# Kernel tuning notes

Measured on AMD Instinct MI355X. Metric: run time of the kernel, lower is better.

## Reference

```python
import jax, jax.numpy as jnp
import numpy as np

BATCH, SEQ, FEAT, UNITS, OUT = 128, 2048, 64, 64, 6


def setup_inputs() -> dict:
    key = jax.random.key(0)
    ks = jax.random.split(key, 12)
    s = 0.05
    inp = {
        "x": jax.random.normal(ks[0], (BATCH, SEQ, FEAT), dtype=jnp.float32),
        # LSTMCell 0 (kernel, recurrent_kernel, bias); gate order i,f,g,o
        "W0": jax.random.normal(ks[1], (FEAT, 4 * UNITS), dtype=jnp.float32) * s,
        "U0": jax.random.normal(ks[2], (UNITS, 4 * UNITS), dtype=jnp.float32) * s,
        "b0": jax.random.normal(ks[3], (4 * UNITS,), dtype=jnp.float32) * s,
        # LSTMCell 1 (shared by layers 2 AND 3, as in the original code)
        "W1": jax.random.normal(ks[4], (UNITS, 4 * UNITS), dtype=jnp.float32) * s,
        "U1": jax.random.normal(ks[5], (UNITS, 4 * UNITS), dtype=jnp.float32) * s,
        "b1": jax.random.normal(ks[6], (4 * UNITS,), dtype=jnp.float32) * s,
        # Dense heads
        "Wf": jax.random.normal(ks[7], (UNITS, 64), dtype=jnp.float32) * s,
        "bf": jax.random.normal(ks[8], (64,), dtype=jnp.float32) * s,
        "Wo": jax.random.normal(ks[9], (64, OUT), dtype=jnp.float32) * s,
        "bo": jax.random.normal(ks[10], (OUT,), dtype=jnp.float32) * s,
    }
    return inp


def _lstm_cell(c, h, xin, W, U, b):
    # Keras LSTMCell math, gate order i, f, g(candidate), o
    z = xin @ W + h @ U + b  # [B, 4U]
    i, f, g, o = jnp.split(z, 4, axis=-1)
    c_new = jax.nn.sigmoid(f) * c + jax.nn.sigmoid(i) * jnp.tanh(g)
    h_new = jax.nn.sigmoid(o) * jnp.tanh(c_new)
    return c_new, h_new


def reference(x, W0, U0, b0, W1, U1, b1, Wf, bf, Wo, bo):
    B = x.shape[0]
    z = jnp.zeros((B, UNITS), dtype=x.dtype)
    init = (z, z, z, z, z, z)  # (c0,h0,c1,h1,c2,h2)

    def step(carry, xt):
        c0, h0, c1, h1, c2, h2 = carry
        c0, h0 = _lstm_cell(c0, h0, xt, W0, U0, b0)
        c1, h1 = _lstm_cell(c1, h1, h0, W1, U1, b1)
        # NOTE: original code reuses rnn_cell1's weights for the 3rd layer
        c2, h2 = _lstm_cell(c2, h2, h1, W1, U1, b1)
        return (c0, h0, c1, h1, c2, h2), None

    xt = jnp.swapaxes(x, 0, 1)  # [T, B, F]
    (c0, h0, c1, h1, c2, h2), _ = jax.lax.scan(step, init, xt)
    y = jax.nn.relu(h2 @ Wf + bf)
    return y @ Wo + bo
```

## Files before the change

### kernel.cpp

```cpp
#include <hip/hip_runtime.h>

#define BATCHN 128
#define SEQT   2048
#define FEAT   64
#define UNITS  64
#define NCOL   256
#define OUTD   6

typedef float v2f __attribute__((ext_vector_type(2)));

__device__ __forceinline__ float fast_exp2(float x) {
#if __has_builtin(__builtin_amdgcn_exp2f)
    return __builtin_amdgcn_exp2f(x);
#else
    return exp2f(x);
#endif
}
__device__ __forceinline__ float fast_rcp(float x) {
#if __has_builtin(__builtin_amdgcn_rcpf)
    return __builtin_amdgcn_rcpf(x);
#else
    return 1.0f / x;
#endif
}
__device__ __forceinline__ float sig_(float x) {
    return fast_rcp(1.0f + fast_exp2(-1.4426950408889634f * x));
}
__device__ __forceinline__ float tanh_(float x) {
    float xc = fminf(fmaxf(x, -15.0f), 15.0f);
    float e  = fast_exp2(2.8853900817779268f * xc);
    return (e - 1.0f) * fast_rcp(e + 1.0f);
}

__device__ __forceinline__ v2f pk_fma(v2f a, v2f b, v2f c) {
    return __builtin_elementwise_fma(a, b, c);
}

template<int CTRL>
__device__ __forceinline__ float dppf(float v) {
    return __builtin_bit_cast(float, __builtin_amdgcn_update_dpp(
        0, __builtin_bit_cast(int, v), CTRL, 0xF, 0xF, true));
}
__device__ __forceinline__ float red4(float v) {
    v += dppf<0xB1>(v);
    v += dppf<0x4E>(v);
    return v;
}

__global__ __launch_bounds__(768, 3)
void lstm3_pipe3(const float* __restrict__ x,
                 const float* __restrict__ W0, const float* __restrict__ U0,
                 const float* __restrict__ b0,
                 const float* __restrict__ W1, const float* __restrict__ U1,
                 const float* __restrict__ b1,
                 const float* __restrict__ Wf, const float* __restrict__ bfv,
                 const float* __restrict__ Wo, const float* __restrict__ bov,
                 float* __restrict__ out)
{
    const int b   = blockIdx.x;
    const int tid = threadIdx.x;
    const int grp = tid >> 8;
    const int lt  = tid & 255;
    const int u   = lt >> 2;
    const int q   = lt & 3;

    __shared__ __align__(16) float lx[2][FEAT];
    __shared__ __align__(16) float lh[3][2][UNITS];
    __shared__ float lact[UNITS];

    const float* Wsel = (grp == 0) ? W0 : W1;
    const float* Usel = (grp == 0) ? U0 : U1;
    const float* bsel = (grp == 0) ? b0 : b1;

    v2f wa[4][8], wb[4][8];
    float bias[4];
#pragma unroll
    for (int g = 0; g < 4; ++g) {
        const int col = (g << 6) + u;
#pragma unroll
        for (int j = 0; j < 8; ++j) {
            const int r = q * 16 + 2 * j;
            wa[g][j] = (v2f){Wsel[r * NCOL + col], Wsel[(r + 1) * NCOL + col]};
            wb[g][j] = (v2f){Usel[r * NCOL + col], Usel[(r + 1) * NCOL + col]};
        }
        bias[g] = bsel[col];
    }

    if (tid < 3 * 2 * UNITS) ((float*)lh)[tid] = 0.f;
    const float* xbase = x + (size_t)b * SEQT * FEAT;
    const bool xload = (grp == 0) && (lt < 16);
    if (xload)
        *(float4*)&lx[1][lt * 4] = *(const float4*)(xbase + lt * 4);
    __syncthreads();

    const float* inP0 = (grp == 0) ? &lx[0][q * 16] : &lh[grp - 1][0][q * 16];
    const float* inP1 = (grp == 0) ? &lx[1][q * 16] : &lh[grp - 1][1][q * 16];
    const float* rcP0 = &lh[grp][0][q * 16];
    const float* rcP1 = &lh[grp][1][q * 16];

    float c = 0.f;

    for (int tk = 0; tk < SEQT + 2; ++tk) {
        const int p = tk & 1;
        const int t = tk - grp;
        const bool active = (t >= 0) && (t < SEQT);

        float4 xg;
        const bool loading = xload && (tk + 1 < SEQT);
        if (loading)
            xg = *(const float4*)(xbase + (size_t)(tk + 1) * FEAT + lt * 4);

        if (active) {
            const float* inP = p ? inP0 : inP1;
            const float* rcP = p ? rcP0 : rcP1;

            v2f acc[4];
#pragma unroll
            for (int g = 0; g < 4; ++g) acc[g] = (v2f){0.f, 0.f};

#pragma unroll
            for (int kc = 0; kc < 4; ++kc) {
                float4 iv = *(const float4*)(inP + kc * 4);
                v2f i0 = (v2f){iv.x, iv.y}, i1 = (v2f){iv.z, iv.w};
#pragma unroll
                for (int g = 0; g < 4; ++g) {
                    acc[g] = pk_fma(i0, wa[g][2 * kc],     acc[g]);
                    acc[g] = pk_fma(i1, wa[g][2 * kc + 1], acc[g]);
                }
            }
#pragma unroll
            for (int kc = 0; kc < 4; ++kc) {
                float4 rv = *(const float4*)(rcP + kc * 4);
                v2f r0 = (v2f){rv.x, rv.y}, r1 = (v2f){rv.z, rv.w};
#pragma unroll
                for (int g = 0; g < 4; ++g) {
                    acc[g] = pk_fma(r0, wb[g][2 * kc],     acc[g]);
                    acc[g] = pk_fma(r1, wb[g][2 * kc + 1], acc[g]);
                }
            }

            float z[4];
#pragma unroll
            for (int g = 0; g < 4; ++g)
                z[g] = red4(acc[g].x + acc[g].y) + bias[g];

            float ig = sig_(z[0]), fg = sig_(z[1]);
            float gg = tanh_(z[2]), og = sig_(z[3]);
            c = fg * c + ig * gg;
            float hn = og * tanh_(c);
            if (q == 0) lh[grp][p][u] = hn;
        }

        if (loading)
            *(float4*)&lx[p][lt * 4] = xg;

        __syncthreads();
    }

    const float* h2f = lh[2][1];
    if (tid < UNITS) {
        float acc = bfv[tid];
#pragma unroll
        for (int k = 0; k < UNITS; ++k) acc += h2f[k] * Wf[k * 64 + tid];
        lact[tid] = fmaxf(acc, 0.f);
    }
    __syncthreads();
    if (tid < OUTD) {
        float acc = bov[tid];
#pragma unroll
        for (int k = 0; k < UNITS; ++k) acc += lact[k] * Wo[k * OUTD + tid];
        out[b * OUTD + tid] = acc;
    }
}

extern "C" void kernel_launch(void* const* d_in, const int* in_sizes, int n_in,
                              void* d_out, int out_size, void* d_ws, size_t ws_size,
                              hipStream_t stream) {
    const float* x   = (const float*)d_in[0];
    const float* W0  = (const float*)d_in[1];
    const float* U0  = (const float*)d_in[2];
    const float* b0  = (const float*)d_in[3];
    const float* W1  = (const float*)d_in[4];
    const float* U1  = (const float*)d_in[5];
    const float* b1  = (const float*)d_in[6];
    const float* Wf  = (const float*)d_in[7];
    const float* bfv = (const float*)d_in[8];
    const float* Wo  = (const float*)d_in[9];
    const float* bov = (const float*)d_in[10];
    float* out = (float*)d_out;

    lstm3_pipe3<<<BATCHN, 768, 0, stream>>>(x, W0, U0, b0, W1, U1, b1,
                                            Wf, bfv, Wo, bov, out);
}
```

Baseline: 2.053 ms.

## Repartition gate matvec to 8-lane groups with two units per group

Each group of 8 lanes now computes two hidden units. Four lanes take the input-weight half and four take the recurrent half, each covering 16 rows of K, with packed FMAs over adjacent column pairs. The reduction becomes a 3-step DPP over 8 lanes on v2f, and shared memory is re-laid out into padded 20-float chunks so the wider per-lane reads avoid bank conflicts. This is meant to cut the per-lane LDS read count and the redundant reductions per step, at the cost of an extra DPP step, a row-broadcast DPP (0x141) whose correctness across 8 lanes is uncertain, and duplicated gate math for both units.

```diff
diff --git a/kernel.cpp b/kernel.cpp
--- a/kernel.cpp
+++ b/kernel.cpp
@@ -6,6 +6,8 @@
 #define UNITS  64
 #define NCOL   256
 #define OUTD   6
+#define CH     20
+#define BUF    96
 
 typedef float v2f __attribute__((ext_vector_type(2)));
 
@@ -41,62 +43,74 @@
     return __builtin_bit_cast(float, __builtin_amdgcn_update_dpp(
         0, __builtin_bit_cast(int, v), CTRL, 0xF, 0xF, true));
 }
-__device__ __forceinline__ float red4(float v) {
-    v += dppf<0xB1>(v);
-    v += dppf<0x4E>(v);
+__device__ __forceinline__ v2f red8v(v2f v) {
+    v2f t;
+    t.x = dppf<0xB1>(v.x);  t.y = dppf<0xB1>(v.y);  v = v + t;
+    t.x = dppf<0x4E>(v.x);  t.y = dppf<0x4E>(v.y);  v = v + t;
+    t.x = dppf<0x141>(v.x); t.y = dppf<0x141>(v.y); v = v + t;
     return v;
 }
 
 __global__ __launch_bounds__(768, 3)
-void lstm3_pipe3(const float* __restrict__ x,
-                 const float* __restrict__ W0, const float* __restrict__ U0,
-                 const float* __restrict__ b0,
-                 const float* __restrict__ W1, const float* __restrict__ U1,
-                 const float* __restrict__ b1,
-                 const float* __restrict__ Wf, const float* __restrict__ bfv,
-                 const float* __restrict__ Wo, const float* __restrict__ bov,
-                 float* __restrict__ out)
+void lstm3_g8(const float* __restrict__ x,
+              const float* __restrict__ W0, const float* __restrict__ U0,
+              const float* __restrict__ b0,
+              const float* __restrict__ W1, const float* __restrict__ U1,
+              const float* __restrict__ b1,
+              const float* __restrict__ Wf, const float* __restrict__ bfv,
+              const float* __restrict__ Wo, const float* __restrict__ bov,
+              float* __restrict__ out)
 {
     const int b   = blockIdx.x;
     const int tid = threadIdx.x;
     const int grp = tid >> 8;
     const int lt  = tid & 255;
-    const int u   = lt >> 2;
-    const int q   = lt & 3;
-
-    __shared__ __align__(16) float lx[2][FEAT];
-    __shared__ __align__(16) float lh[3][2][UNITS];
+    const int cg  = lt >> 3;
+    const int kg  = lt & 7;
+    const int up  = kg & 1;
+    const int myu = 2 * cg + up;
+
+    __shared__ __align__(16) float ls[8 * BUF];
     __shared__ float lact[UNITS];
+    float* const lsb = ls;
 
     const float* Wsel = (grp == 0) ? W0 : W1;
     const float* Usel = (grp == 0) ? U0 : U1;
     const float* bsel = (grp == 0) ? b0 : b1;
-
-    v2f wa[4][8], wb[4][8];
-    float bias[4];
+    const float* Msel = (kg < 4) ? Wsel : Usel;
+
+    v2f wt[16][4];
+    float biasv[4];
 #pragma unroll
     for (int g = 0; g < 4; ++g) {
-        const int col = (g << 6) + u;
-#pragma unroll
-        for (int j = 0; j < 8; ++j) {
-            const int r = q * 16 + 2 * j;
-            wa[g][j] = (v2f){Wsel[r * NCOL + col], Wsel[(r + 1) * NCOL + col]};
-            wb[g][j] = (v2f){Usel[r * NCOL + col], Usel[(r + 1) * NCOL + col]};
+        const int colb = (g << 6) + 2 * cg;
+#pragma unroll
+        for (int k = 0; k < 16; ++k) {
+            const int r = (kg & 3) * 16 + k;
+            wt[k][g] = (v2f){Msel[r * NCOL + colb], Msel[r * NCOL + colb + 1]};
         }
-        bias[g] = bsel[col];
-    }
-
-    if (tid < 3 * 2 * UNITS) ((float*)lh)[tid] = 0.f;
+        biasv[g] = bsel[(g << 6) + myu];
+    }
+
+    if (tid < 6 * BUF) lsb[tid] = 0.f;
+
     const float* xbase = x + (size_t)b * SEQT * FEAT;
     const bool xload = (grp == 0) && (lt < 16);
-    if (xload)
-        *(float4*)&lx[1][lt * 4] = *(const float4*)(xbase + lt * 4);
+    float* xwp0 = lsb + 6 * BUF + CH * (lt >> 2) + 4 * (lt & 3);
+    float* xwp1 = xwp0 + BUF;
+    if (xload) *(float4*)xwp1 = *(const float4*)(xbase + lt * 4);
     __syncthreads();
 
-    const float* inP0 = (grp == 0) ? &lx[0][q * 16] : &lh[grp - 1][0][q * 16];
-    const float* inP1 = (grp == 0) ? &lx[1][q * 16] : &lh[grp - 1][1][q * 16];
-    const float* rcP0 = &lh[grp][0][q * 16];
-    const float* rcP1 = &lh[grp][1][q * 16];
+    const float* inB0 = (grp == 0) ? (lsb + 6 * BUF) : (lsb + (2 * (grp - 1) + 0) * BUF);
+    const float* inB1 = inB0 + BUF;
+    const float* rcB0 = lsb + (2 * grp + 0) * BUF;
+    const float* rcB1 = rcB0 + BUF;
+    const int chOff = (kg & 3) * CH;
+    const float* opP0 = ((kg < 4) ? inB0 : rcB0) + chOff;
+    const float* opP1 = ((kg < 4) ? inB1 : rcB1) + chOff;
+
+    float* hwp0 = lsb + (2 * grp + 0) * BUF + CH * (myu >> 4) + (myu & 15);
+    float* hwp1 = hwp0 + BUF;
 
     float c = 0.f;
 
@@ -111,65 +125,67 @@
             xg = *(const float4*)(xbase + (size_t)(tk + 1) * FEAT + lt * 4);
 
         if (active) {
-            const float* inP = p ? inP0 : inP1;
-            const float* rcP = p ? rcP0 : rcP1;
+            const float* op = p ? opP0 : opP1;
+            float4 o0 = *(const float4*)(op);
+            float4 o1 = *(const float4*)(op + 4);
+            float4 o2 = *(const float4*)(op + 8);
+            float4 o3 = *(const float4*)(op + 12);
 
             v2f acc[4];
 #pragma unroll
             for (int g = 0; g < 4; ++g) acc[g] = (v2f){0.f, 0.f};
 
-#pragma unroll
-            for (int kc = 0; kc < 4; ++kc) {
-                float4 iv = *(const float4*)(inP + kc * 4);
-                v2f i0 = (v2f){iv.x, iv.y}, i1 = (v2f){iv.z, iv.w};
-#pragma unroll
-                for (int g = 0; g < 4; ++g) {
-                    acc[g] = pk_fma(i0, wa[g][2 * kc],     acc[g]);
-                    acc[g] = pk_fma(i1, wa[g][2 * kc + 1], acc[g]);
-                }
+#define MAC(V, K)                                                     \
+            {                                                         \
+                v2f s = (v2f){(V), (V)};                              \
+                acc[0] = pk_fma(s, wt[K][0], acc[0]);                 \
+                acc[1] = pk_fma(s, wt[K][1], acc[1]);                 \
+                acc[2] = pk_fma(s, wt[K][2], acc[2]);                 \
+                acc[3] = pk_fma(s, wt[K][3], acc[3]);                 \
             }
-#pragma unroll
-            for (int kc = 0; kc < 4; ++kc) {
-                float4 rv = *(const float4*)(rcP + kc * 4);
-                v2f r0 = (v2f){rv.x, rv.y}, r1 = (v2f){rv.z, rv.w};
-#pragma unroll
-                for (int g = 0; g < 4; ++g) {
-                    acc[g] = pk_fma(r0, wb[g][2 * kc],     acc[g]);
-                    acc[g] = pk_fma(r1, wb[g][2 * kc + 1], acc[g]);
-                }
-            }
-
-            float z[4];
-#pragma unroll
-            for (int g = 0; g < 4; ++g)
-                z[g] = red4(acc[g].x + acc[g].y) + bias[g];
-
-            float ig = sig_(z[0]), fg = sig_(z[1]);
-            float gg = tanh_(z[2]), og = sig_(z[3]);
+            MAC(o0.x, 0)  MAC(o0.y, 1)  MAC(o0.z, 2)  MAC(o0.w, 3)
+            MAC(o1.x, 4)  MAC(o1.y, 5)  MAC(o1.z, 6)  MAC(o1.w, 7)
+            MAC(o2.x, 8)  MAC(o2.y, 9)  MAC(o2.z, 10) MAC(o2.w, 11)
+            MAC(o3.x, 12) MAC(o3.y, 13) MAC(o3.z, 14) MAC(o3.w, 15)
+#undef MAC
+
+            v2f z0 = red8v(acc[0]);
+            v2f z1 = red8v(acc[1]);
+            v2f z2 = red8v(acc[2]);
+            v2f z3 = red8v(acc[3]);
+
+            const float zi = (up ? z0.y : z0.x) + biasv[0];
+            const float zf = (up ? z1.y : z1.x) + biasv[1];
+            const float zg = (up ? z2.y : z2.x) + biasv[2];
+            const float zo = (up ? z3.y : z3.x) + biasv[3];
+
+            const float ig = sig_(zi), fg = sig_(zf);
+            const float gg = tanh_(zg), og = sig_(zo);
             c = fg * c + ig * gg;
-            float hn = og * tanh_(c);
-            if (q == 0) lh[grp][p][u] = hn;
+            const float hn = og * tanh_(c);
+            if (kg < 2) *(p ? hwp1 : hwp0) = hn;
         }
 
         if (loading)
-            *(float4*)&lx[p][lt * 4] = xg;
+            *(float4*)(p ? xwp1 : xwp0) = xg;
 
         __syncthreads();
     }
 
-    const float* h2f = lh[2][1];
+    const float* h2f = lsb + (2 * 2 + 1) * BUF;
     if (tid < UNITS) {
-        float acc = bfv[tid];
-#pragma unroll
-        for (int k = 0; k < UNITS; ++k) acc += h2f[k] * Wf[k * 64 + tid];
-        lact[tid] = fmaxf(acc, 0.f);
+        float a = bfv[tid];
+#pragma unroll
+        for (int k = 0; k < UNITS; ++k)
+            a += h2f[CH * (k >> 4) + (k & 15)] * Wf[k * 64 + tid];
+        lact[tid] = fmaxf(a, 0.f);
     }
     __syncthreads();
     if (tid < OUTD) {
-        float acc = bov[tid];
-#pragma unroll
-        for (int k = 0; k < UNITS; ++k) acc += lact[k] * Wo[k * OUTD + tid];
-        out[b * OUTD + tid] = acc;
+        float a = bov[tid];
+#pragma unroll
+        for (int k = 0; k < UNITS; ++k) a += lact[k] * Wo[k * OUTD + tid];
+        out[b * OUTD + tid] = a;
     }
 }
 
@@ -189,6 +205,6 @@
     const float* bov = (const float*)d_in[10];
     float* out = (float*)d_out;
 
-    lstm3_pipe3<<<BATCHN, 768, 0, stream>>>(x, W0, U0, b0, W1, U1, b1,
-                                            Wf, bfv, Wo, bov, out);
-}
+    lstm3_g8<<<BATCHN, 768, 0, stream>>>(x, W0, U0, b0, W1, U1, b1,
+                                         Wf, bfv, Wo, bov, out);
+}
```

Measured after the change: 2.006 ms. 2.3% less time.
